# Optimization experiments

Measured on AMD Instinct MI355X. Metric: run time of the kernel, lower is better.

## Reference

```python
import jax, jax.numpy as jnp
import numpy as np

EMBED_SIZE = 1024
HEADS = 16
HEAD_DIM = EMBED_SIZE // HEADS
N, L = 2, 2048


def setup_inputs() -> dict:
    key = jax.random.key(0)
    ks = jax.random.split(key, 6)
    values = jax.random.normal(ks[0], (N, L, EMBED_SIZE), dtype=jnp.float32)
    keys_t = jax.random.normal(ks[1], (N, L, EMBED_SIZE), dtype=jnp.float32)
    query = jax.random.normal(ks[2], (N, L, EMBED_SIZE), dtype=jnp.float32)
    mask = jax.random.randint(ks[3], (N, 1, L, L), 0, 2, dtype=jnp.int32)
    # fc_out params (torch Linear: y = x @ W.T + b)
    Wo = jax.random.normal(ks[4], (EMBED_SIZE, EMBED_SIZE), dtype=jnp.float32) * (EMBED_SIZE ** -0.5)
    bo = jax.random.normal(ks[5], (EMBED_SIZE,), dtype=jnp.float32) * 0.01
    return {"values": values, "keys": keys_t, "query": query, "mask": mask, "Wo": Wo, "bo": bo}


def reference(values, keys, query, mask, Wo, bo):
    # NOTE: the original torch module defines per-head q/k/v Linears but never
    # calls them in forward; only fc_out is applied. We reproduce that exactly.
    n, q_len, _ = query.shape
    v = values.reshape(n, -1, HEADS, HEAD_DIM)   # nkhd
    k = keys.reshape(n, -1, HEADS, HEAD_DIM)     # nkhd
    q = query.reshape(n, q_len, HEADS, HEAD_DIM) # nqhd
    energy = jnp.einsum('nqhd,nkhd->nhqk', q, k)
    energy = jnp.where(mask == 0, jnp.float32(-1e20), energy)
    scale = jnp.float32(EMBED_SIZE) ** 0.5  # sqrt(embed_size), as in source
    attn = jax.nn.softmax(energy / scale, axis=3)
    out = jnp.einsum('nhqk,nkhd->nqhd', attn, v).reshape(n, q_len, HEADS * HEAD_DIM)
    return out @ Wo.T + bo
```

## Files before the change

### kernel.cpp

```cpp
#include <hip/hip_runtime.h>
#include <hip/hip_bf16.h>
#include <stdint.h>

#define LSEQ 2048
#define NBATCH 2
#define NHEADS 16
#define HDIM 64
#define EMB 1024

typedef __bf16 bf16x8 __attribute__((ext_vector_type(8)));
typedef float f32x4 __attribute__((ext_vector_type(4)));
typedef unsigned short ushort4v __attribute__((ext_vector_type(4)));
typedef unsigned short ushort8v __attribute__((ext_vector_type(8)));

#define QSCALE (1.44269504088896f / 32.0f)

static __device__ __forceinline__ unsigned short f2bf(float f) {
  union { float f; uint32_t u; } v; v.f = f;
  uint32_t u = v.u;
  u += 0x7fffu + ((u >> 16) & 1u);
  return (unsigned short)(u >> 16);
}

static __device__ __forceinline__ f32x4 mfma16(bf16x8 a, bf16x8 b, f32x4 c) {
  return __builtin_amdgcn_mfma_f32_16x16x32_bf16(a, b, c, 0, 0, 0);
}

static __device__ __forceinline__ float mexp2(float e, uint32_t m, int b) {
  uint32_t keep = (uint32_t)__builtin_amdgcn_sbfe((int)m, b, 1);
  return __uint_as_float(__float_as_uint(__builtin_amdgcn_exp2f(e)) & keep);
}

__global__ __launch_bounds__(256) void prep_kernel(
    const float* __restrict__ q, const float* __restrict__ k,
    const float* __restrict__ w, const int* __restrict__ mask,
    const float* __restrict__ v,
    unsigned short* __restrict__ qb, unsigned short* __restrict__ kb,
    unsigned short* __restrict__ wb, unsigned char* __restrict__ mb8,
    unsigned short* __restrict__ vt) {
  int b = blockIdx.x;
  if (b < 8192) {
    int idx = b * 256 + threadIdx.x;
    const float* src; unsigned short* dst; int t; int swz;
    if (idx < (1 << 20)) { src = q; dst = qb; t = idx; swz = 0; }
    else                 { src = k; dst = kb; t = idx - (1 << 20); swz = 1; }
    int e = t << 2;
    int d = e & 63;
    int h = (e >> 6) & 15;
    int l = (e >> 10) & (LSEQ - 1);
    int n = e >> 21;
    float4 vv = reinterpret_cast<const float4*>(src)[t];
    int dd = d;
    if (swz) dd = ((((d >> 3) ^ (l & 7)) << 3) | (d & 7));
    else { vv.x *= QSCALE; vv.y *= QSCALE; vv.z *= QSCALE; vv.w *= QSCALE; }
    ushort4v o;
    o.x = f2bf(vv.x); o.y = f2bf(vv.y); o.z = f2bf(vv.z); o.w = f2bf(vv.w);
    size_t oi = (((size_t)n * NHEADS + h) * LSEQ + l) * HDIM + dd;
    *reinterpret_cast<ushort4v*>(dst + oi) = o;
  } else if (b < 9216) {
    int t = (b - 8192) * 256 + threadIdx.x;
    float4 vv = reinterpret_cast<const float4*>(w)[t];
    ushort4v o;
    o.x = f2bf(vv.x); o.y = f2bf(vv.y); o.z = f2bf(vv.z); o.w = f2bf(vv.w);
    reinterpret_cast<ushort4v*>(wb)[t] = o;
  } else if (b < 13312) {
    int idx = (b - 9216) * 256 + threadIdx.x;
    const int* mp = mask + (size_t)idx * 8;
    int4 m0 = *reinterpret_cast<const int4*>(mp);
    int4 m1 = *reinterpret_cast<const int4*>(mp + 4);
    unsigned int bb = (m0.x ? 1u : 0u) | (m0.y ? 2u : 0u) | (m0.z ? 4u : 0u) |
                      (m0.w ? 8u : 0u) | (m1.x ? 16u : 0u) | (m1.y ? 32u : 0u) |
                      (m1.z ? 64u : 0u) | (m1.w ? 128u : 0u);
    mb8[idx] = (unsigned char)bb;
  } else {
    int b2 = b - 13312;
    int kc = b2 & 63;
    int h  = (b2 >> 6) & 15;
    int n  = b2 >> 10;
    int t  = threadIdx.x;
    int d    = t & 63;
    int sgrp = t >> 6;
    const float* src = v + (size_t)n * LSEQ * EMB + h * HDIM + d;
    ushort8v o;
#pragma unroll
    for (int j = 0; j < 8; ++j) {
      int kp = (j < 4) ? (4 * sgrp + j) : (16 + 4 * sgrp + (j - 4));
      float f = src[(size_t)(kc * 32 + kp) * EMB];
      o[j] = f2bf(f);
    }
    int cs = sgrp ^ ((d >> 1) & 3);
    size_t base = (((size_t)(n * NHEADS + h) * 64 + kc) * HDIM + d) * 32 + (cs << 3);
    *reinterpret_cast<ushort8v*>(vt + base) = o;
  }
}

__global__ __launch_bounds__(512, 4) void attn_kernel(
    const unsigned short* __restrict__ Kb, const unsigned short* __restrict__ Qb,
    const unsigned short* __restrict__ VT, const uint32_t* __restrict__ maskw,
    unsigned short* __restrict__ Op) {
  __shared__ unsigned short lds[2][16384];

  int bid = blockIdx.x;
  bid = (bid & 7) * 64 + (bid >> 3);
  int qt = bid & 15;
  int h  = (bid >> 4) & 15;
  int n  = bid >> 8;
  int tid  = threadIdx.x;
  int wave = tid >> 6;
  int lane = tid & 63;
  int g  = lane >> 4;
  int qi = lane & 15;
  int qrow = qt * 128 + wave * 16 + qi;

  const unsigned short* qptr = Qb + (((size_t)n * NHEADS + h) * LSEQ + qrow) * HDIM;
  bf16x8 bq0 = *reinterpret_cast<const bf16x8*>(qptr + g * 8);
  bf16x8 bq1 = *reinterpret_cast<const bf16x8*>(qptr + 32 + g * 8);

  const unsigned short* khead  = Kb + (((size_t)n * NHEADS + h) * LSEQ) * HDIM;
  const unsigned short* vthead = VT + ((size_t)(n * NHEADS + h) * 64) * (HDIM * 32);
  const uint32_t* mrow = maskw + ((size_t)n * LSEQ + qrow) * 64;

  int xk = qi & 7;
  int kA = qi * 64 + ((g ^ xk) << 3);
  int kB = qi * 64 + (((4 + g) ^ xk) << 3);
  int kC = kA + 1024;
  int kD = kB + 1024;
  int xv = (qi >> 1) & 3;
  int vA = qi * 32 + ((g ^ xv) << 3);

  union { uint32_t u[4]; bf16x8 v; } ones;
  ones.u[0] = 0x3F803F80u; ones.u[1] = 0x3F803F80u;
  ones.u[2] = 0x3F803F80u; ones.u[3] = 0x3F803F80u;

  f32x4 z = {0.f, 0.f, 0.f, 0.f};
  f32x4 acc0 = z, acc1 = z, acc2 = z, acc3 = z;
  f32x4 sacc = z;

#define STAGE(T, BUF) do {                                                     \
    const unsigned short* kg_ = khead  + (size_t)(T) * 8192 + tid * 8;         \
    const unsigned short* vg_ = vthead + (size_t)(T) * 8192 + tid * 8;         \
    _Pragma("unroll")                                                          \
    for (int j_ = 0; j_ < 2; ++j_) {                                           \
      __builtin_amdgcn_global_load_lds(                                        \
          (const __attribute__((address_space(1))) uint32_t*)(kg_ + j_ * 4096),\
          (__attribute__((address_space(3))) uint32_t*)                        \
              &lds[BUF][j_ * 4096 + wave * 512],                               \
          16, 0, 0);                                                           \
      __builtin_amdgcn_global_load_lds(                                        \
          (const __attribute__((address_space(1))) uint32_t*)(vg_ + j_ * 4096),\
          (__attribute__((address_space(3))) uint32_t*)                        \
              &lds[BUF][8192 + j_ * 4096 + wave * 512],                        \
          16, 0, 0);                                                           \
    }                                                                          \
  } while (0)

#define COMPUTE(BUF, CH, MW) do {                                              \
    const unsigned short* lk_ = &lds[BUF][(CH) * 2048];                        \
    const unsigned short* lv_ = &lds[BUF][8192 + (CH) * 2048];                 \
    bf16x8 K0 = *(const bf16x8*)(lk_ + kA);                                    \
    bf16x8 K1 = *(const bf16x8*)(lk_ + kB);                                    \
    bf16x8 K2 = *(const bf16x8*)(lk_ + kC);                                    \
    bf16x8 K3 = *(const bf16x8*)(lk_ + kD);                                    \
    f32x4 e0 = z, e1 = z;                                                      \
    e0 = mfma16(K0, bq0, e0); e0 = mfma16(K1, bq1, e0);                        \
    e1 = mfma16(K2, bq0, e1); e1 = mfma16(K3, bq1, e1);                        \
    bf16x8 V0 = *(const bf16x8*)(lv_ + vA);                                    \
    bf16x8 V1 = *(const bf16x8*)(lv_ + vA + 512);                              \
    bf16x8 V2 = *(const bf16x8*)(lv_ + vA + 1024);                             \
    bf16x8 V3 = *(const bf16x8*)(lv_ + vA + 1536);                             \
    uint32_t m0_ = (MW) >> (4 * g);                                            \
    uint32_t m1_ = (MW) >> (16 + 4 * g);                                       \
    float p0 = mexp2(e0[0], m0_, 0);                                           \
    float p1 = mexp2(e0[1], m0_, 1);                                           \
    float p2 = mexp2(e0[2], m0_, 2);                                           \
    float p3 = mexp2(e0[3], m0_, 3);                                           \
    float p4 = mexp2(e1[0], m1_, 0);                                           \
    float p5 = mexp2(e1[1], m1_, 1);                                           \
    float p6 = mexp2(e1[2], m1_, 2);                                           \
    float p7 = mexp2(e1[3], m1_, 3);                                           \
    union { uint32_t u[4]; bf16x8 v; } pf;                                     \
    asm("v_cvt_pk_bf16_f32 %0, %1, %2" : "=v"(pf.u[0]) : "v"(p0), "v"(p1));    \
    asm("v_cvt_pk_bf16_f32 %0, %1, %2" : "=v"(pf.u[1]) : "v"(p2), "v"(p3));    \
    asm("v_cvt_pk_bf16_f32 %0, %1, %2" : "=v"(pf.u[2]) : "v"(p4), "v"(p5));    \
    asm("v_cvt_pk_bf16_f32 %0, %1, %2" : "=v"(pf.u[3]) : "v"(p6), "v"(p7));    \
    acc0 = mfma16(V0, pf.v, acc0);                                             \
    acc1 = mfma16(V1, pf.v, acc1);                                             \
    acc2 = mfma16(V2, pf.v, acc2);                                             \
    acc3 = mfma16(V3, pf.v, acc3);                                             \
    sacc = mfma16(ones.v, pf.v, sacc);                                         \
  } while (0)

  uint4 mw0 = *(const uint4*)(mrow);
  uint4 mw1, mw2;
  STAGE(0, 0);
  __syncthreads();

  for (int t = 0; t < 16; t += 2) {
    int t1 = (t + 1) & 15;
    mw1 = *(const uint4*)(mrow + 4 * t1);
    STAGE(t1, 1);
    COMPUTE(0, 0, mw0.x);
    COMPUTE(0, 1, mw0.y);
    COMPUTE(0, 2, mw0.z);
    COMPUTE(0, 3, mw0.w);
    __syncthreads();
    int t2 = (t + 2) & 15;
    mw2 = *(const uint4*)(mrow + 4 * t2);
    STAGE(t2, 0);
    COMPUTE(1, 0, mw1.x);
    COMPUTE(1, 1, mw1.y);
    COMPUTE(1, 2, mw1.z);
    COMPUTE(1, 3, mw1.w);
    __syncthreads();
    mw0 = mw2;
  }
#undef STAGE
#undef COMPUTE

  float inv = 1.0f / sacc[0];

  size_t ob = ((size_t)n * LSEQ + qrow) * EMB + h * HDIM;
  ushort4v s0, s1, s2, s3;
#pragma unroll
  for (int r = 0; r < 4; ++r) {
    s0[r] = f2bf(acc0[r] * inv);
    s1[r] = f2bf(acc1[r] * inv);
    s2[r] = f2bf(acc2[r] * inv);
    s3[r] = f2bf(acc3[r] * inv);
  }
  *reinterpret_cast<ushort4v*>(Op + ob + 0  + 4 * g) = s0;
  *reinterpret_cast<ushort4v*>(Op + ob + 16 + 4 * g) = s1;
  *reinterpret_cast<ushort4v*>(Op + ob + 32 + 4 * g) = s2;
  *reinterpret_cast<ushort4v*>(Op + ob + 48 + 4 * g) = s3;
}

__global__ __launch_bounds__(256, 2) void proj_kernel(
    const unsigned short* __restrict__ A, const unsigned short* __restrict__ B,
    const float* __restrict__ bo, float* __restrict__ out) {
  __shared__ unsigned short plds[2][6144];

  int bid = blockIdx.x;
  bid = (bid & 7) * 64 + (bid >> 3);
  int mb0 = (bid >> 4) * 128;
  int nb0 = (bid & 15) * 64;
  int tid  = threadIdx.x;
  int wave = tid >> 6;
  int lane = tid & 63;
  int g  = lane >> 4;
  int qi = lane & 15;
  int wm = wave >> 1, wn = wave & 1;

  int srow = tid >> 2;
  int scol = (((tid & 3) ^ ((tid >> 3) & 3)) << 3);
  const unsigned short* aS0 = A + (size_t)(mb0 + srow) * EMB + scol;
  const unsigned short* aS1 = aS0 + (size_t)64 * EMB;
  const unsigned short* bS  = B + (size_t)(nb0 + srow) * EMB + scol;

  int xa = (qi >> 1) & 3;
  int gof = ((g ^ xa) << 3);
  int aof0 = (wm * 64 + qi) * 32 + gof;
  int aof1 = aof0 + 16 * 32;
  int aof2 = aof0 + 32 * 32;
  int aof3 = aof0 + 48 * 32;
  int bof0 = (wn * 32 + qi) * 32 + gof;
  int bof1 = bof0 + 16 * 32;

  f32x4 z = {0.f, 0.f, 0.f, 0.f};
  f32x4 acc00 = z, acc01 = z, acc10 = z, acc11 = z;
  f32x4 acc20 = z, acc21 = z, acc30 = z, acc31 = z;

#define PSTAGE(KT, BUF) do {                                                   \
    __builtin_amdgcn_global_load_lds(                                          \
        (const __attribute__((address_space(1))) uint32_t*)(aS0 + (KT) * 32),  \
        (__attribute__((address_space(3))) uint32_t*)&plds[BUF][wave * 512],   \
        16, 0, 0);                                                             \
    __builtin_amdgcn_global_load_lds(                                          \
        (const __attribute__((address_space(1))) uint32_t*)(aS1 + (KT) * 32),  \
        (__attribute__((address_space(3))) uint32_t*)&plds[BUF][2048 + wave * 512], \
        16, 0, 0);                                                             \
    __builtin_amdgcn_global_load_lds(                                          \
        (const __attribute__((address_space(1))) uint32_t*)(bS + (KT) * 32),   \
        (__attribute__((address_space(3))) uint32_t*)&plds[BUF][4096 + wave * 512], \
        16, 0, 0);                                                             \
  } while (0)

#define PCOMPUTE(BUF) do {                                                     \
    const unsigned short* la_ = &plds[BUF][0];                                 \
    const unsigned short* lb_ = &plds[BUF][4096];                              \
    bf16x8 a0 = *(const bf16x8*)(la_ + aof0);                                  \
    bf16x8 a1 = *(const bf16x8*)(la_ + aof1);                                  \
    bf16x8 a2 = *(const bf16x8*)(la_ + aof2);                                  \
    bf16x8 a3 = *(const bf16x8*)(la_ + aof3);                                  \
    bf16x8 b0 = *(const bf16x8*)(lb_ + bof0);                                  \
    bf16x8 b1 = *(const bf16x8*)(lb_ + bof1);                                  \
    acc00 = mfma16(a0, b0, acc00); acc01 = mfma16(a0, b1, acc01);              \
    acc10 = mfma16(a1, b0, acc10); acc11 = mfma16(a1, b1, acc11);              \
    acc20 = mfma16(a2, b0, acc20); acc21 = mfma16(a2, b1, acc21);              \
    acc30 = mfma16(a3, b0, acc30); acc31 = mfma16(a3, b1, acc31);              \
  } while (0)

  PSTAGE(0, 0);
  __syncthreads();
  for (int kt = 0; kt < 32; kt += 2) {
    PSTAGE(kt + 1, 1);
    PCOMPUTE(0);
    __syncthreads();
    PSTAGE((kt + 2) & 31, 0);
    PCOMPUTE(1);
    __syncthreads();
  }
#undef PSTAGE
#undef PCOMPUTE

  int orow = mb0 + wm * 64 + 4 * g;
  int col0 = nb0 + wn * 32 + qi;
  float bia0 = bo[col0];
  float bia1 = bo[col0 + 16];
#define PSTORE(ACC0, ACC1, M) do {                                             \
    _Pragma("unroll")                                                          \
    for (int r = 0; r < 4; ++r) {                                              \
      size_t rw = (size_t)(orow + (M) * 16 + r) * EMB;                         \
      out[rw + col0]      = ACC0[r] + bia0;                                    \
      out[rw + col0 + 16] = ACC1[r] + bia1;                                    \
    }                                                                          \
  } while (0)
  PSTORE(acc00, acc01, 0);
  PSTORE(acc10, acc11, 1);
  PSTORE(acc20, acc21, 2);
  PSTORE(acc30, acc31, 3);
#undef PSTORE
}

extern "C" void kernel_launch(void* const* d_in, const int* in_sizes, int n_in,
                              void* d_out, int out_size, void* d_ws, size_t ws_size,
                              hipStream_t stream) {
  const float* Vf   = (const float*)d_in[0];
  const float* Kf   = (const float*)d_in[1];
  const float* Qf   = (const float*)d_in[2];
  const int*   Mask = (const int*)d_in[3];
  const float* Wo   = (const float*)d_in[4];
  const float* Bo   = (const float*)d_in[5];
  float* out = (float*)d_out;

  char* ws = (char*)d_ws;
  unsigned short* Qb  = (unsigned short*)(ws);
  unsigned short* Kb  = (unsigned short*)(ws + (size_t)8  * 1024 * 1024);
  unsigned short* VTb = (unsigned short*)(ws + (size_t)16 * 1024 * 1024);
  unsigned short* Wob = (unsigned short*)(ws + (size_t)24 * 1024 * 1024);
  unsigned short* Opb = (unsigned short*)(ws + (size_t)26 * 1024 * 1024);
  unsigned char*  Mb  = (unsigned char*)(ws + (size_t)34 * 1024 * 1024);

  prep_kernel<<<15360, 256, 0, stream>>>(Qf, Kf, Wo, Mask, Vf, Qb, Kb, Wob, Mb, VTb);
  attn_kernel<<<512, 512, 0, stream>>>(Kb, Qb, VTb, (const uint32_t*)Mb, Opb);
  proj_kernel<<<512, 256, 0, stream>>>(Opb, Wob, Bo, out);
}
```

Measured before the change: 83.92 us.

## Raise wave priority around attention MFMA and double K-step per projection stage

The attention loop raises wave scheduling priority with s_setprio around each compute block, so MFMA-issuing waves are favoured over waves issuing loads. The output projection kernel doubles its LDS buffers and stages two K-slices per barrier, which halves the number of __syncthreads in the GEMM main loop. The cost is twice the shared memory per block in the projection kernel (48 KB with two blocks per CU), which could limit occupancy.

```diff
diff --git a/kernel.cpp b/kernel.cpp
--- a/kernel.cpp
+++ b/kernel.cpp
@@ -199,18 +199,22 @@
     int t1 = (t + 1) & 15;
     mw1 = *(const uint4*)(mrow + 4 * t1);
     STAGE(t1, 1);
+    __builtin_amdgcn_s_setprio(1);
     COMPUTE(0, 0, mw0.x);
     COMPUTE(0, 1, mw0.y);
     COMPUTE(0, 2, mw0.z);
     COMPUTE(0, 3, mw0.w);
+    __builtin_amdgcn_s_setprio(0);
     __syncthreads();
     int t2 = (t + 2) & 15;
     mw2 = *(const uint4*)(mrow + 4 * t2);
     STAGE(t2, 0);
+    __builtin_amdgcn_s_setprio(1);
     COMPUTE(1, 0, mw1.x);
     COMPUTE(1, 1, mw1.y);
     COMPUTE(1, 2, mw1.z);
     COMPUTE(1, 3, mw1.w);
+    __builtin_amdgcn_s_setprio(0);
     __syncthreads();
     mw0 = mw2;
   }
@@ -237,7 +241,7 @@
 __global__ __launch_bounds__(256, 2) void proj_kernel(
     const unsigned short* __restrict__ A, const unsigned short* __restrict__ B,
     const float* __restrict__ bo, float* __restrict__ out) {
-  __shared__ unsigned short plds[2][6144];
+  __shared__ unsigned short plds[2][12288];
 
   int bid = blockIdx.x;
   bid = (bid & 7) * 64 + (bid >> 3);
@@ -269,24 +273,31 @@
   f32x4 acc00 = z, acc01 = z, acc10 = z, acc11 = z;
   f32x4 acc20 = z, acc21 = z, acc30 = z, acc31 = z;
 
-#define PSTAGE(KT, BUF) do {                                                   \
-    __builtin_amdgcn_global_load_lds(                                          \
-        (const __attribute__((address_space(1))) uint32_t*)(aS0 + (KT) * 32),  \
-        (__attribute__((address_space(3))) uint32_t*)&plds[BUF][wave * 512],   \
-        16, 0, 0);                                                             \
-    __builtin_amdgcn_global_load_lds(                                          \
-        (const __attribute__((address_space(1))) uint32_t*)(aS1 + (KT) * 32),  \
-        (__attribute__((address_space(3))) uint32_t*)&plds[BUF][2048 + wave * 512], \
-        16, 0, 0);                                                             \
-    __builtin_amdgcn_global_load_lds(                                          \
-        (const __attribute__((address_space(1))) uint32_t*)(bS + (KT) * 32),   \
-        (__attribute__((address_space(3))) uint32_t*)&plds[BUF][4096 + wave * 512], \
-        16, 0, 0);                                                             \
-  } while (0)
-
-#define PCOMPUTE(BUF) do {                                                     \
-    const unsigned short* la_ = &plds[BUF][0];                                 \
-    const unsigned short* lb_ = &plds[BUF][4096];                              \
+#define PSTAGE2(KT, BUF) do {                                                  \
+    _Pragma("unroll")                                                          \
+    for (int p_ = 0; p_ < 2; ++p_) {                                           \
+      int kt_ = ((KT) + p_) & 31;                                              \
+      __builtin_amdgcn_global_load_lds(                                        \
+          (const __attribute__((address_space(1))) uint32_t*)(aS0 + kt_ * 32), \
+          (__attribute__((address_space(3))) uint32_t*)                        \
+              &plds[BUF][p_ * 6144 + wave * 512],                              \
+          16, 0, 0);                                                           \
+      __builtin_amdgcn_global_load_lds(                                        \
+          (const __attribute__((address_space(1))) uint32_t*)(aS1 + kt_ * 32), \
+          (__attribute__((address_space(3))) uint32_t*)                        \
+              &plds[BUF][p_ * 6144 + 2048 + wave * 512],                       \
+          16, 0, 0);                                                           \
+      __builtin_amdgcn_global_load_lds(                                        \
+          (const __attribute__((address_space(1))) uint32_t*)(bS + kt_ * 32),  \
+          (__attribute__((address_space(3))) uint32_t*)                        \
+              &plds[BUF][p_ * 6144 + 4096 + wave * 512],                       \
+          16, 0, 0);                                                           \
+    }                                                                          \
+  } while (0)
+
+#define PCOMPUTE(BUF, P) do {                                                  \
+    const unsigned short* la_ = &plds[BUF][(P) * 6144];                        \
+    const unsigned short* lb_ = &plds[BUF][(P) * 6144 + 4096];                 \
     bf16x8 a0 = *(const bf16x8*)(la_ + aof0);                                  \
     bf16x8 a1 = *(const bf16x8*)(la_ + aof1);                                  \
     bf16x8 a2 = *(const bf16x8*)(la_ + aof2);                                  \
@@ -299,17 +310,19 @@
     acc30 = mfma16(a3, b0, acc30); acc31 = mfma16(a3, b1, acc31);              \
   } while (0)
 
-  PSTAGE(0, 0);
+  PSTAGE2(0, 0);
   __syncthreads();
-  for (int kt = 0; kt < 32; kt += 2) {
-    PSTAGE(kt + 1, 1);
-    PCOMPUTE(0);
+  for (int kt = 0; kt < 32; kt += 4) {
+    PSTAGE2(kt + 2, 1);
+    PCOMPUTE(0, 0);
+    PCOMPUTE(0, 1);
     __syncthreads();
-    PSTAGE((kt + 2) & 31, 0);
-    PCOMPUTE(1);
+    PSTAGE2((kt + 4) & 31, 0);
+    PCOMPUTE(1, 0);
+    PCOMPUTE(1, 1);
     __syncthreads();
   }
-#undef PSTAGE
+#undef PSTAGE2
 #undef PCOMPUTE
 
   int orow = mb0 + wm * 64 + 4 * g;
```

Measured after the change: 82.69 us. No clear change (-1.5%).
